# Kernel optimization log

Hardware: AMD Instinct MI355X
Metric: run time of the kernel (lower is better)

## Reference

```python
import jax, jax.numpy as jnp
import numpy as np

GRID = 3  # 3x3 grid; with H=W=168 and center_hw=56 all patches are 56x56


def setup_inputs() -> dict:
    key = jax.random.key(0)
    k1, k2, k3, k4 = jax.random.split(key, 4)
    B, C, H, W = 8, 256, 168, 168
    d = C // 8
    x = jax.random.normal(k1, (B, C, H, W), dtype=jnp.float32)
    W_B = jax.random.normal(k2, (d, C), dtype=jnp.float32) * 0.05
    W_D = jax.random.normal(k3, (d, C), dtype=jnp.float32) * 0.05
    W_phi = jax.random.normal(k4, (C, d), dtype=jnp.float32) * 0.05
    return {"x": x, "W_B": W_B, "W_D": W_D, "W_phi": W_phi}


def _psnl(fflat, W_B, W_D, W_phi):
    # fflat: [P, C, n] flattened patches; low-rank (non-softmax) path
    n = fflat.shape[-1]
    d = W_B.shape[0]
    Bn = jnp.einsum('dc,pcn->pnd', W_B, fflat)   # to_B, [P,n,d]
    Dn = jnp.einsum('dc,pcn->pnd', W_D, fflat)   # to_D
    Bc = Bn - jnp.mean(Bn, axis=1, keepdims=True)  # mean-center over positions
    T = jnp.einsum('pnd,pne->pde', Bc, Dn) / jnp.float32(n)  # [P,d,d]
    U = jnp.einsum('pnd,pde->pne', Bc, T)        # [P,n,d]
    out = jnp.einsum('cd,pnd->pcn', W_phi, U)    # phi 1x1 conv
    return out + fflat


def reference(x, W_B, W_D, W_phi):
    B, C, H, W = x.shape
    ph, pw = H // GRID, W // GRID
    n = ph * pw
    # split into 3x3 equal patches: [B,C,H,W] -> [B*9, C, n]
    xp = x.reshape(B, C, GRID, ph, GRID, pw)
    xp = xp.transpose(0, 2, 4, 1, 3, 5).reshape(B * GRID * GRID, C, n)
    yp = _psnl(xp, W_B, W_D, W_phi)
    # reassemble
    y = yp.reshape(B, GRID, GRID, C, ph, pw).transpose(0, 3, 1, 4, 2, 5)
    return y.reshape(B, C, H, W)
```

## Files before the change

kernel.cpp:

```cpp
#include <hip/hip_runtime.h>


#define BB    8
#define CC    256
#define HH    168
#define WWs   168
#define HWs   28224
#define PH    56
#define NPOS  3136
#define NP    72
#define DD    32

#define OFF_WBT 0
#define OFF_WDT (OFF_WBT + 8192)
#define OFF_BN  (OFF_WDT + 8192)
#define OFF_DN  (OFF_BN + 7225344)
#define OFF_SP  (OFF_DN + 7225344)
#define OFF_MBP (OFF_SP + 72*8*1024)
#define OFF_MDP (OFF_MBP + 72*8*32)
#define OFF_G   (OFF_MDP + 72*8*32)
#define OFF_H   (OFF_G + 72*256*32)

__global__ void ktrans(const float* __restrict__ wb, const float* __restrict__ wd,
                       float* __restrict__ wbt, float* __restrict__ wdt) {
    const int c = threadIdx.x;
    #pragma unroll
    for (int d = 0; d < DD; ++d) {
        wbt[c * DD + d] = wb[d * CC + c];
        wdt[c * DD + d] = wd[d * CC + c];
    }
}

__global__ __launch_bounds__(256) void kA(const float* __restrict__ x,
                                          const float* __restrict__ wbt,
                                          const float* __restrict__ wdt,
                                          float* __restrict__ bn,
                                          float* __restrict__ dn) {
    const int jb = blockIdx.x;
    const int p  = blockIdx.y;
    const int t  = threadIdx.x;
    const int j  = jb * 256 + t;
    const bool valid = j < NPOS;
    const int jc = valid ? j : (NPOS - 1);
    const int b  = p / 9;
    const int gy = (p % 9) / 3;
    const int gx = p % 3;
    const int iy = jc / PH;
    const int ix = jc % PH;
    const long base = (long)b * CC * HWs + (long)(gy * PH + iy) * WWs + (gx * PH + ix);

    float accB[DD], accD[DD];
    #pragma unroll
    for (int d = 0; d < DD; ++d) { accB[d] = 0.f; accD[d] = 0.f; }

    const float* xc = x + base;
    #pragma unroll 1
    for (int c0 = 0; c0 < CC; c0 += 8) {
        float xv[8];
        #pragma unroll
        for (int u = 0; u < 8; ++u) xv[u] = xc[(long)u * HWs];
        #pragma unroll
        for (int u = 0; u < 8; ++u) {
            const float* wbp = wbt + (c0 + u) * DD;
            const float* wdp = wdt + (c0 + u) * DD;
            #pragma unroll
            for (int d = 0; d < DD; ++d) {
                accB[d] = fmaf(xv[u], wbp[d], accB[d]);
                accD[d] = fmaf(xv[u], wdp[d], accD[d]);
            }
        }
        xc += 8L * HWs;
    }

    if (valid) {
        float* bp = bn + (long)p * DD * NPOS + j;
        float* dp = dn + (long)p * DD * NPOS + j;
        #pragma unroll
        for (int d = 0; d < DD; ++d) {
            bp[(long)d * NPOS] = accB[d];
            dp[(long)d * NPOS] = accD[d];
        }
    }
}

#define B1_TJ 56
__global__ __launch_bounds__(256) void kB1(const float* __restrict__ bn,
                                           const float* __restrict__ dn,
                                           float* __restrict__ spart,
                                           float* __restrict__ mbp,
                                           float* __restrict__ mdp) {
    const int qb = blockIdx.x;
    const int p  = blockIdx.y;
    const int t  = threadIdx.x;
    const int j0 = qb * 392;
    __shared__ float Bt[B1_TJ][34];
    __shared__ float Dt[B1_TJ][34];
    const int d2 = (t >> 4) << 1;
    const int e2 = (t & 15) << 1;
    float a00 = 0, a01 = 0, a10 = 0, a11 = 0;
    float mb0 = 0, mb1 = 0, md0 = 0, md1 = 0;

    const long pbase = (long)p * DD * NPOS;
    for (int tt = 0; tt < 7; ++tt) {
        const int jt = j0 + tt * B1_TJ;
        __syncthreads();
        for (int i = t; i < B1_TJ * DD; i += 256) {
            const int d  = i / B1_TJ;
            const int jj = i % B1_TJ;
            Bt[jj][d] = bn[pbase + (long)d * NPOS + jt + jj];
            Dt[jj][d] = dn[pbase + (long)d * NPOS + jt + jj];
        }
        __syncthreads();
        #pragma unroll 4
        for (int jj = 0; jj < B1_TJ; ++jj) {
            const float2 bv = *(const float2*)&Bt[jj][d2];
            const float2 dv = *(const float2*)&Dt[jj][e2];
            a00 = fmaf(bv.x, dv.x, a00);
            a01 = fmaf(bv.x, dv.y, a01);
            a10 = fmaf(bv.y, dv.x, a10);
            a11 = fmaf(bv.y, dv.y, a11);
            if (e2 == 0) { mb0 += bv.x; mb1 += bv.y; }
            if (d2 == 0) { md0 += dv.x; md1 += dv.y; }
        }
    }

    float* sp = spart + (long)(p * 8 + qb) * 1024;
    sp[(d2    ) * DD + e2    ] = a00;
    sp[(d2    ) * DD + e2 + 1] = a01;
    sp[(d2 + 1) * DD + e2    ] = a10;
    sp[(d2 + 1) * DD + e2 + 1] = a11;
    if (e2 == 0) { mbp[(p * 8 + qb) * DD + d2] = mb0; mbp[(p * 8 + qb) * DD + d2 + 1] = mb1; }
    if (d2 == 0) { mdp[(p * 8 + qb) * DD + e2] = md0; mdp[(p * 8 + qb) * DD + e2 + 1] = md1; }
}

__global__ __launch_bounds__(256) void kB2(const float* __restrict__ wphi,
                                           const float* __restrict__ spart,
                                           const float* __restrict__ mbp,
                                           const float* __restrict__ mdp,
                                           float* __restrict__ gout,
                                           float* __restrict__ hout) {
    const int p = blockIdx.x;
    const int t = threadIdx.x;
    __shared__ float Tm[DD][DD + 1];
    __shared__ float mbs[DD], mds[DD];

    if (t < DD) {
        float s1 = 0, s2 = 0;
        for (int q = 0; q < 8; ++q) {
            s1 += mbp[(p * 8 + q) * DD + t];
            s2 += mdp[(p * 8 + q) * DD + t];
        }
        mbs[t] = s1; mds[t] = s2;
    }
    __syncthreads();

    const float invn = 1.0f / (float)NPOS;
    {
        float4 s = make_float4(0.f, 0.f, 0.f, 0.f);
        for (int q = 0; q < 8; ++q) {
            const float4 v = *(const float4*)&spart[(long)(p * 8 + q) * 1024 + t * 4];
            s.x += v.x; s.y += v.y; s.z += v.z; s.w += v.w;
        }
        const int idx = t * 4;
        const int d = idx >> 5;
        const int e = idx & 31;
        const float mbd = mbs[d] * invn;
        Tm[d][e    ] = s.x * invn - mbd * (mds[e    ] * invn);
        Tm[d][e + 1] = s.y * invn - mbd * (mds[e + 1] * invn);
        Tm[d][e + 2] = s.z * invn - mbd * (mds[e + 2] * invn);
        Tm[d][e + 3] = s.w * invn - mbd * (mds[e + 3] * invn);
    }
    __syncthreads();

    const int c = t;
    float wp[DD];
    #pragma unroll
    for (int e = 0; e < DD; ++e) wp[e] = wphi[c * DD + e];
    float h = 0.f;
    float* gp = gout + ((long)p * CC + c) * DD;
    #pragma unroll 4
    for (int d = 0; d < DD; ++d) {
        float g = 0.f;
        #pragma unroll
        for (int e = 0; e < DD; ++e) g = fmaf(wp[e], Tm[d][e], g);
        gp[d] = g;
        h = fmaf(mbs[d] * invn, g, h);
    }
    hout[p * CC + c] = h;
}

__global__ __launch_bounds__(256) void kC(const float* __restrict__ x,
                                          const float* __restrict__ bn,
                                          const float* __restrict__ gbuf,
                                          const float* __restrict__ hbuf,
                                          float* __restrict__ out) {
    const int jb = blockIdx.x;
    const int p  = blockIdx.y;
    const int t  = threadIdx.x;
    const int j  = jb * 256 + t;
    const bool valid = j < NPOS;
    const int jc = valid ? j : (NPOS - 1);
    const int b  = p / 9;
    const int gy = (p % 9) / 3;
    const int gx = p % 3;
    const int iy = jc / PH;
    const int ix = jc % PH;
    const long base = (long)b * CC * HWs + (long)(gy * PH + iy) * WWs + (gx * PH + ix);

    float bnv[DD];
    const float* bp = bn + (long)p * DD * NPOS + jc;
    #pragma unroll
    for (int d = 0; d < DD; ++d) bnv[d] = bp[(long)d * NPOS];

    const float* gp = gbuf + (long)p * CC * DD;
    const float* hp = hbuf + p * CC;
    const float* xc = x + base;
    float* oc = out + base;
    #pragma unroll 1
    for (int c0 = 0; c0 < CC; c0 += 8) {
        float xv[8];
        #pragma unroll
        for (int u = 0; u < 8; ++u) xv[u] = xc[(long)u * HWs];
        #pragma unroll
        for (int u = 0; u < 8; ++u) {
            float acc = -hp[c0 + u];
            const float* g = gp + (c0 + u) * DD;
            #pragma unroll
            for (int d = 0; d < DD; ++d) acc = fmaf(bnv[d], g[d], acc);
            if (valid) oc[(long)u * HWs] = xv[u] + acc;
        }
        xc += 8L * HWs;
        oc += 8L * HWs;
    }
}

extern "C" void kernel_launch(void* const* d_in, const int* in_sizes, int n_in,
                              void* d_out, int out_size, void* d_ws, size_t ws_size,
                              hipStream_t stream) {
    const float* x    = (const float*)d_in[0];
    const float* wb   = (const float*)d_in[1];
    const float* wd   = (const float*)d_in[2];
    const float* wphi = (const float*)d_in[3];
    float* ws = (float*)d_ws;

    float* wbt = ws + OFF_WBT;
    float* wdt = ws + OFF_WDT;
    float* bnp = ws + OFF_BN;
    float* dnp = ws + OFF_DN;
    float* sp  = ws + OFF_SP;
    float* mbp = ws + OFF_MBP;
    float* mdp = ws + OFF_MDP;
    float* gb  = ws + OFF_G;
    float* hb  = ws + OFF_H;

    hipLaunchKernelGGL(ktrans, dim3(1), dim3(256), 0, stream, wb, wd, wbt, wdt);
    hipLaunchKernelGGL(kA, dim3(13, 72), dim3(256), 0, stream, x, wbt, wdt, bnp, dnp);
    hipLaunchKernelGGL(kB1, dim3(8, 72), dim3(256), 0, stream, bnp, dnp, sp, mbp, mdp);
    hipLaunchKernelGGL(kB2, dim3(72), dim3(256), 0, stream, wphi, sp, mbp, mdp, gb, hb);
    hipLaunchKernelGGL(kC, dim3(13, 72), dim3(256), 0, stream, x, bnp, gb, hb, (float*)d_out);
}
```

Measured before the change: 592.7 us.

## Fuse projection with Gram reduction and split output kernel over channel halves

The B/D projection kernel now reduces its results into per-block partial d×d Gram sums and column means directly from registers through shared memory. This removes the Dn buffer and the separate pass that reread Bn and Dn from global memory. The reduction now produces 13 partials per patch instead of 8, and kB2 sums over that count. The output kernel also gains a z-dimension that splits the 256 channels into two halves, doubling its block count for more parallelism at the cost of reloading Bn twice.

```diff
diff --git a/kernel.cpp b/kernel.cpp
--- a/kernel.cpp
+++ b/kernel.cpp
@@ -10,16 +10,16 @@
 #define NPOS  3136
 #define NP    72
 #define DD    32
+#define NPART 13
 
 #define OFF_WBT 0
 #define OFF_WDT (OFF_WBT + 8192)
 #define OFF_BN  (OFF_WDT + 8192)
-#define OFF_DN  (OFF_BN + 7225344)
-#define OFF_SP  (OFF_DN + 7225344)
-#define OFF_MBP (OFF_SP + 72*8*1024)
-#define OFF_MDP (OFF_MBP + 72*8*32)
-#define OFF_G   (OFF_MDP + 72*8*32)
-#define OFF_H   (OFF_G + 72*256*32)
+#define OFF_SP  (OFF_BN + 7225344)
+#define OFF_MBP (OFF_SP + 958464)
+#define OFF_MDP (OFF_MBP + 29952)
+#define OFF_G   (OFF_MDP + 29952)
+#define OFF_H   (OFF_G + 589824)
 
 __global__ void ktrans(const float* __restrict__ wb, const float* __restrict__ wd,
                        float* __restrict__ wbt, float* __restrict__ wdt) {
@@ -31,11 +31,13 @@
     }
 }
 
-__global__ __launch_bounds__(256) void kA(const float* __restrict__ x,
-                                          const float* __restrict__ wbt,
-                                          const float* __restrict__ wdt,
-                                          float* __restrict__ bn,
-                                          float* __restrict__ dn) {
+__global__ __launch_bounds__(256) void kAB(const float* __restrict__ x,
+                                           const float* __restrict__ wbt,
+                                           const float* __restrict__ wdt,
+                                           float* __restrict__ bn,
+                                           float* __restrict__ spart,
+                                           float* __restrict__ mbp,
+                                           float* __restrict__ mdp) {
     const int jb = blockIdx.x;
     const int p  = blockIdx.y;
     const int t  = threadIdx.x;
@@ -72,47 +74,36 @@
         xc += 8L * HWs;
     }
 
-    if (valid) {
+    if (!valid) {
+        #pragma unroll
+        for (int d = 0; d < DD; ++d) { accB[d] = 0.f; accD[d] = 0.f; }
+    } else {
         float* bp = bn + (long)p * DD * NPOS + j;
-        float* dp = dn + (long)p * DD * NPOS + j;
-        #pragma unroll
-        for (int d = 0; d < DD; ++d) {
-            bp[(long)d * NPOS] = accB[d];
-            dp[(long)d * NPOS] = accD[d];
-        }
-    }
-}
-
-#define B1_TJ 56
-__global__ __launch_bounds__(256) void kB1(const float* __restrict__ bn,
-                                           const float* __restrict__ dn,
-                                           float* __restrict__ spart,
-                                           float* __restrict__ mbp,
-                                           float* __restrict__ mdp) {
-    const int qb = blockIdx.x;
-    const int p  = blockIdx.y;
-    const int t  = threadIdx.x;
-    const int j0 = qb * 392;
-    __shared__ float Bt[B1_TJ][34];
-    __shared__ float Dt[B1_TJ][34];
+        #pragma unroll
+        for (int d = 0; d < DD; ++d) bp[(long)d * NPOS] = accB[d];
+    }
+
+    __shared__ float Bt[128][33];
+    __shared__ float Dt[128][33];
     const int d2 = (t >> 4) << 1;
     const int e2 = (t & 15) << 1;
     float a00 = 0, a01 = 0, a10 = 0, a11 = 0;
     float mb0 = 0, mb1 = 0, md0 = 0, md1 = 0;
 
-    const long pbase = (long)p * DD * NPOS;
-    for (int tt = 0; tt < 7; ++tt) {
-        const int jt = j0 + tt * B1_TJ;
+    #pragma unroll 1
+    for (int r = 0; r < 2; ++r) {
         __syncthreads();
-        for (int i = t; i < B1_TJ * DD; i += 256) {
-            const int d  = i / B1_TJ;
-            const int jj = i % B1_TJ;
-            Bt[jj][d] = bn[pbase + (long)d * NPOS + jt + jj];
-            Dt[jj][d] = dn[pbase + (long)d * NPOS + jt + jj];
+        if ((t >> 7) == r) {
+            const int tr = t & 127;
+            #pragma unroll
+            for (int d = 0; d < DD; ++d) {
+                Bt[tr][d] = accB[d];
+                Dt[tr][d] = accD[d];
+            }
         }
         __syncthreads();
         #pragma unroll 4
-        for (int jj = 0; jj < B1_TJ; ++jj) {
+        for (int jj = 0; jj < 128; ++jj) {
             const float2 bv = *(const float2*)&Bt[jj][d2];
             const float2 dv = *(const float2*)&Dt[jj][e2];
             a00 = fmaf(bv.x, dv.x, a00);
@@ -124,13 +115,13 @@
         }
     }
 
-    float* sp = spart + (long)(p * 8 + qb) * 1024;
+    float* sp = spart + (long)(p * NPART + jb) * 1024;
     sp[(d2    ) * DD + e2    ] = a00;
     sp[(d2    ) * DD + e2 + 1] = a01;
     sp[(d2 + 1) * DD + e2    ] = a10;
     sp[(d2 + 1) * DD + e2 + 1] = a11;
-    if (e2 == 0) { mbp[(p * 8 + qb) * DD + d2] = mb0; mbp[(p * 8 + qb) * DD + d2 + 1] = mb1; }
-    if (d2 == 0) { mdp[(p * 8 + qb) * DD + e2] = md0; mdp[(p * 8 + qb) * DD + e2 + 1] = md1; }
+    if (e2 == 0) { mbp[(p * NPART + jb) * DD + d2] = mb0; mbp[(p * NPART + jb) * DD + d2 + 1] = mb1; }
+    if (d2 == 0) { mdp[(p * NPART + jb) * DD + e2] = md0; mdp[(p * NPART + jb) * DD + e2 + 1] = md1; }
 }
 
 __global__ __launch_bounds__(256) void kB2(const float* __restrict__ wphi,
@@ -146,9 +137,9 @@
 
     if (t < DD) {
         float s1 = 0, s2 = 0;
-        for (int q = 0; q < 8; ++q) {
-            s1 += mbp[(p * 8 + q) * DD + t];
-            s2 += mdp[(p * 8 + q) * DD + t];
+        for (int q = 0; q < NPART; ++q) {
+            s1 += mbp[(p * NPART + q) * DD + t];
+            s2 += mdp[(p * NPART + q) * DD + t];
         }
         mbs[t] = s1; mds[t] = s2;
     }
@@ -157,8 +148,8 @@
     const float invn = 1.0f / (float)NPOS;
     {
         float4 s = make_float4(0.f, 0.f, 0.f, 0.f);
-        for (int q = 0; q < 8; ++q) {
-            const float4 v = *(const float4*)&spart[(long)(p * 8 + q) * 1024 + t * 4];
+        for (int q = 0; q < NPART; ++q) {
+            const float4 v = *(const float4*)&spart[(long)(p * NPART + q) * 1024 + t * 4];
             s.x += v.x; s.y += v.y; s.z += v.z; s.w += v.w;
         }
         const int idx = t * 4;
@@ -196,6 +187,7 @@
                                           float* __restrict__ out) {
     const int jb = blockIdx.x;
     const int p  = blockIdx.y;
+    const int cbase = blockIdx.z * 128;
     const int t  = threadIdx.x;
     const int j  = jb * 256 + t;
     const bool valid = j < NPOS;
@@ -205,19 +197,20 @@
     const int gx = p % 3;
     const int iy = jc / PH;
     const int ix = jc % PH;
-    const long base = (long)b * CC * HWs + (long)(gy * PH + iy) * WWs + (gx * PH + ix);
+    const long base = (long)b * CC * HWs + (long)(gy * PH + iy) * WWs + (gx * PH + ix)
+                    + (long)cbase * HWs;
 
     float bnv[DD];
     const float* bp = bn + (long)p * DD * NPOS + jc;
     #pragma unroll
     for (int d = 0; d < DD; ++d) bnv[d] = bp[(long)d * NPOS];
 
-    const float* gp = gbuf + (long)p * CC * DD;
-    const float* hp = hbuf + p * CC;
+    const float* gp = gbuf + (long)p * CC * DD + (long)cbase * DD;
+    const float* hp = hbuf + p * CC + cbase;
     const float* xc = x + base;
     float* oc = out + base;
     #pragma unroll 1
-    for (int c0 = 0; c0 < CC; c0 += 8) {
+    for (int c0 = 0; c0 < 128; c0 += 8) {
         float xv[8];
         #pragma unroll
         for (int u = 0; u < 8; ++u) xv[u] = xc[(long)u * HWs];
@@ -246,7 +239,6 @@
     float* wbt = ws + OFF_WBT;
     float* wdt = ws + OFF_WDT;
     float* bnp = ws + OFF_BN;
-    float* dnp = ws + OFF_DN;
     float* sp  = ws + OFF_SP;
     float* mbp = ws + OFF_MBP;
     float* mdp = ws + OFF_MDP;
@@ -254,8 +246,7 @@
     float* hb  = ws + OFF_H;
 
     hipLaunchKernelGGL(ktrans, dim3(1), dim3(256), 0, stream, wb, wd, wbt, wdt);
-    hipLaunchKernelGGL(kA, dim3(13, 72), dim3(256), 0, stream, x, wbt, wdt, bnp, dnp);
-    hipLaunchKernelGGL(kB1, dim3(8, 72), dim3(256), 0, stream, bnp, dnp, sp, mbp, mdp);
+    hipLaunchKernelGGL(kAB, dim3(13, 72), dim3(256), 0, stream, x, wbt, wdt, bnp, sp, mbp, mdp);
     hipLaunchKernelGGL(kB2, dim3(72), dim3(256), 0, stream, wphi, sp, mbp, mdp, gb, hb);
-    hipLaunchKernelGGL(kC, dim3(13, 72), dim3(256), 0, stream, x, bnp, gb, hb, (float*)d_out);
-}
+    hipLaunchKernelGGL(kC, dim3(13, 72, 2), dim3(256), 0, stream, x, bnp, gb, hb, (float*)d_out);
+}
```

Result: slower. 650.0 us (+9.7%).
